# Performance work log

Measured on AMD Instinct MI355X. Metric: run time of the kernel, lower is better.

## Reference

```python
import jax, jax.numpy as jnp
import numpy as np

SHRINK_THRES = 0.0025
EPS = 1e-12  # F.normalize default eps


def _l2norm(v, axis=-1):
    return v / jnp.maximum(jnp.linalg.norm(v, axis=axis, keepdims=True), EPS)


def setup_inputs() -> dict:
    key = jax.random.key(0)
    ks = jax.random.split(key, 5)
    N, C, H, W = 16, 256, 64, 64
    mem_dim = 512
    x = jax.random.normal(ks[0], (N, C, H, W), dtype=jnp.float32)
    memory = jax.random.normal(ks[1], (mem_dim, C), dtype=jnp.float32) * 0.1
    memory = _l2norm(memory, axis=1)
    w1 = jax.random.normal(ks[2], (C, C // 2), dtype=jnp.float32) * (1.0 / np.sqrt(C))
    b1 = jnp.zeros((C // 2,), dtype=jnp.float32)
    w2 = jax.random.normal(ks[3], (C // 2, C), dtype=jnp.float32) * (1.0 / np.sqrt(C // 2))
    b2 = jnp.zeros((C,), dtype=jnp.float32)
    return {"x": x, "memory": memory, "w1": w1, "b1": b1, "w2": w2, "b2": b2}


def reference(x, memory, w1, b1, w2, b2):
    N, C, H, W = x.shape
    # [N,C,H,W] -> [N*H*W, C]
    x_flat = jnp.transpose(x, (0, 2, 3, 1)).reshape(-1, C)
    x_norm = _l2norm(x_flat, axis=1)
    # shared MLP over memory slots: Linear -> ReLU -> Linear -> ReLU
    m = jax.nn.relu(memory @ w1 + b1)
    m = jax.nn.relu(m @ w2 + b2)
    mem_norm = _l2norm(m, axis=1)  # [M, C]
    # cosine similarity + softmax over memory slots
    att = jax.nn.softmax(x_norm @ mem_norm.T, axis=1)  # [N*H*W, M]
    # hard shrink + L1 renormalization
    att = jax.nn.relu(att - SHRINK_THRES)
    att = att / jnp.maximum(jnp.sum(att, axis=1, keepdims=True), EPS)
    out_flat = att @ mem_norm  # [N*H*W, C]
    output = jnp.transpose(out_flat.reshape(N, H, W, C), (0, 3, 1, 2))
    att_map = jnp.transpose(att.reshape(N, H, W, -1), (0, 3, 1, 2))
    return output, att_map
```

## Files before the change

kernel.cpp:

```cpp
#include <hip/hip_runtime.h>
#include <hip/hip_bf16.h>

typedef _Float16 half8 __attribute__((ext_vector_type(8)));
typedef _Float16 half4v __attribute__((ext_vector_type(4)));
typedef float floatx4 __attribute__((ext_vector_type(4)));

#define C_DIM 256
#define M_DIM 512
#define HW 4096
#define TAU 0.0025f
#define LCAP 96

__global__ __launch_bounds__(128) void prep_kernel(
    const float* __restrict__ memory, const float* __restrict__ w1,
    const float* __restrict__ b1, const float* __restrict__ w2,
    const float* __restrict__ b2,
    _Float16* __restrict__ mN, float* __restrict__ mN32)
{
  __shared__ float sm[256];
  __shared__ float sh[128];
  __shared__ float s_part[2];
  __shared__ float s_tot;
  const int r = blockIdx.x;
  const int t = threadIdx.x;
  sm[t]       = memory[r * C_DIM + t];
  sm[t + 128] = memory[r * C_DIM + t + 128];
  __syncthreads();
  float acc = b1[t];
#pragma unroll 8
  for (int c = 0; c < 256; ++c) acc = fmaf(sm[c], w1[c * 128 + t], acc);
  sh[t] = fmaxf(acc, 0.f);
  __syncthreads();
  float o0 = b2[t], o1 = b2[t + 128];
#pragma unroll 8
  for (int k = 0; k < 128; ++k) {
    float h = sh[k];
    o0 = fmaf(h, w2[k * 256 + t], o0);
    o1 = fmaf(h, w2[k * 256 + t + 128], o1);
  }
  o0 = fmaxf(o0, 0.f);
  o1 = fmaxf(o1, 0.f);
  float ss = o0 * o0 + o1 * o1;
#pragma unroll
  for (int off = 32; off >= 1; off >>= 1) ss += __shfl_down(ss, off);
  if ((t & 63) == 0) s_part[t >> 6] = ss;
  __syncthreads();
  if (t == 0) s_tot = s_part[0] + s_part[1];
  __syncthreads();
  const float inv = 1.f / fmaxf(sqrtf(s_tot), 1e-12f);
  const float v0 = o0 * inv, v1 = o1 * inv;
  mN[r * C_DIM + t]        = (_Float16)v0;
  mN[r * C_DIM + t + 128]  = (_Float16)v1;
  mN32[r * C_DIM + t]       = v0;
  mN32[r * C_DIM + t + 128] = v1;
}

__global__ __launch_bounds__(256) void zero_kernel(float* __restrict__ p)
{
  const size_t n4 = (size_t)16 * M_DIM * HW / 4;
  size_t i = (size_t)blockIdx.x * 256 + threadIdx.x;
  const size_t stride = (size_t)gridDim.x * 256;
  const floatx4 z = {0.f, 0.f, 0.f, 0.f};
  for (; i < n4; i += stride) ((floatx4*)p)[i] = z;
}

#define MFMA16(a, b, c) __builtin_amdgcn_mfma_f32_16x16x32_f16(a, b, c, 0, 0, 0)

__global__ __launch_bounds__(512, 4) void main_kernel(
    const float* __restrict__ x,
    const _Float16* __restrict__ mN,
    const float* __restrict__ mN32,
    float* __restrict__ out, float* __restrict__ attmap)
{
  __shared__ _Float16       Xh[64][264];
  __shared__ unsigned short s_lslot[64][LCAP];
  __shared__ float          s_lval[64][LCAP];
  __shared__ int      s_cnt[64];
  __shared__ float    s_sumsq[64];
  __shared__ float    s_sum1[64];
  __shared__ float    s_sum2[64];

  const int tid  = threadIdx.x;
  const int wave = tid >> 6;
  const int lane = tid & 63;
  const int q    = lane >> 4;
  const int c16  = lane & 15;
  const int g    = tid >> 3;
  const int pxq  = tid & 7;

  const int blk = blockIdx.x;
  const int img = blk >> 6;
  const int hw0 = (blk & 63) * 64;
  const float* __restrict__ xb = x + (size_t)img * C_DIM * HW + hw0;

  if (tid < 64) {
    s_sumsq[tid] = 0.f; s_sum1[tid] = 0.f; s_sum2[tid] = 0.f; s_cnt[tid] = 0;
  }
  __syncthreads();

#pragma unroll
  for (int h = 0; h < 2; ++h) {
    floatx4 v[4];
#pragma unroll
    for (int i = 0; i < 4; ++i)
      v[i] = *(const floatx4*)(xb + (size_t)(4 * g + i) * HW + (pxq + 8 * h) * 4);
    float ps[4];
#pragma unroll
    for (int j = 0; j < 4; ++j) {
      const int p = (pxq + 8 * h) * 4 + j;
      half4v hv = {(_Float16)v[0][j], (_Float16)v[1][j], (_Float16)v[2][j], (_Float16)v[3][j]};
      *(half4v*)&Xh[p][4 * g] = hv;
      ps[j] = v[0][j] * v[0][j] + v[1][j] * v[1][j] + v[2][j] * v[2][j] + v[3][j] * v[3][j];
    }
#pragma unroll
    for (int off = 8; off < 64; off <<= 1)
#pragma unroll
      for (int j = 0; j < 4; ++j) ps[j] += __shfl_xor(ps[j], off);
    if ((lane >> 3) == 0) {
#pragma unroll
      for (int j = 0; j < 4; ++j) atomicAdd(&s_sumsq[4 * (lane & 7) + 32 * h + j], ps[j]);
    }
  }

  const _Float16* bp[4];
#pragma unroll
  for (int nt = 0; nt < 4; ++nt)
    bp[nt] = mN + (size_t)(wave * 64 + nt * 16 + c16) * C_DIM + q * 8;
  half8 bcur[4], bnxt[4];
#pragma unroll
  for (int nt = 0; nt < 4; ++nt) bcur[nt] = *(const half8*)bp[nt];

  __syncthreads();

  floatx4 acc[4][4];
#pragma unroll
  for (int mt = 0; mt < 4; ++mt)
#pragma unroll
    for (int nt = 0; nt < 4; ++nt) {
      floatx4 z = {0.f, 0.f, 0.f, 0.f};
      acc[mt][nt] = z;
    }
#pragma unroll
  for (int kb = 0; kb < 8; ++kb) {
    if (kb < 7) {
#pragma unroll
      for (int nt = 0; nt < 4; ++nt) bnxt[nt] = *(const half8*)(bp[nt] + (kb + 1) * 32);
    }
    const int k0 = kb * 32 + q * 8;
    half8 ah[4];
#pragma unroll
    for (int mt = 0; mt < 4; ++mt) ah[mt] = *(const half8*)&Xh[mt * 16 + c16][k0];
#pragma unroll
    for (int nt = 0; nt < 4; ++nt)
#pragma unroll
      for (int mt = 0; mt < 4; ++mt)
        acc[mt][nt] = MFMA16(ah[mt], bcur[nt], acc[mt][nt]);
#pragma unroll
    for (int nt = 0; nt < 4; ++nt) bcur[nt] = bnxt[nt];
  }

#pragma unroll
  for (int mt = 0; mt < 4; ++mt)
#pragma unroll
    for (int r = 0; r < 4; ++r) {
      const int m = mt * 16 + q * 4 + r;
      const float iv = 1.f / fmaxf(sqrtf(s_sumsq[m]), 1e-12f);
      float s = 0.f;
#pragma unroll
      for (int nt = 0; nt < 4; ++nt) {
        const float e = __expf(acc[mt][nt][r] * iv);
        acc[mt][nt][r] = e;
        s += e;
      }
      s += __shfl_xor(s, 1);
      s += __shfl_xor(s, 2);
      s += __shfl_xor(s, 4);
      s += __shfl_xor(s, 8);
      if (c16 == 0) atomicAdd(&s_sum1[m], s);
    }
  __syncthreads();

#pragma unroll
  for (int mt = 0; mt < 4; ++mt)
#pragma unroll
    for (int r = 0; r < 4; ++r) {
      const int m = mt * 16 + q * 4 + r;
      const float isum = 1.f / s_sum1[m];
      float s = 0.f;
#pragma unroll
      for (int nt = 0; nt < 4; ++nt) {
        const float tv = fmaxf(acc[mt][nt][r] * isum - TAU, 0.f);
        acc[mt][nt][r] = tv;
        s += tv;
      }
      s += __shfl_xor(s, 1);
      s += __shfl_xor(s, 2);
      s += __shfl_xor(s, 4);
      s += __shfl_xor(s, 8);
      if (c16 == 0) atomicAdd(&s_sum2[m], s);
    }
  __syncthreads();

#pragma unroll
  for (int mt = 0; mt < 4; ++mt) {
    float rs[4];
#pragma unroll
    for (int r = 0; r < 4; ++r)
      rs[r] = 1.f / fmaxf(s_sum2[mt * 16 + q * 4 + r], 1e-12f);
#pragma unroll
    for (int nt = 0; nt < 4; ++nt) {
      floatx4 a4 = acc[mt][nt];
      const unsigned n = wave * 64 + nt * 16 + c16;
#pragma unroll
      for (int r = 0; r < 4; ++r) {
        a4[r] *= rs[r];
        if (a4[r] > 0.f) {
          const int m = mt * 16 + q * 4 + r;
          const int idx = atomicAdd(&s_cnt[m], 1);
          if (idx < LCAP) {
            s_lslot[m][idx] = (unsigned short)n;
            s_lval[m][idx]  = a4[r];
          }
          attmap[((size_t)img * M_DIM + n) * HW + hw0 + m] = a4[r];
        }
      }
    }
  }
  __syncthreads();

  const int px  = lane;
  const int chc = wave;
  const int cn  = min(s_cnt[px], LCAP);
  floatx4 f[8] = {{0.f,0.f,0.f,0.f},{0.f,0.f,0.f,0.f},{0.f,0.f,0.f,0.f},{0.f,0.f,0.f,0.f},
                  {0.f,0.f,0.f,0.f},{0.f,0.f,0.f,0.f},{0.f,0.f,0.f,0.f},{0.f,0.f,0.f,0.f}};
  for (int j = 0; j < cn; ++j) {
    const int slot  = s_lslot[px][j];
    const float v   = s_lval[px][j];
    const floatx4* row = (const floatx4*)(mN32 + (size_t)slot * C_DIM + chc * 32);
#pragma unroll
    for (int u = 0; u < 8; ++u) f[u] += v * row[u];
  }

#pragma unroll
  for (int cc = 0; cc < 32; ++cc)
    out[((size_t)img * C_DIM + chc * 32 + cc) * HW + hw0 + px] = f[cc >> 2][cc & 3];
}

extern "C" void kernel_launch(void* const* d_in, const int* in_sizes, int n_in,
                              void* d_out, int out_size, void* d_ws, size_t ws_size,
                              hipStream_t stream) {
  (void)in_sizes; (void)n_in; (void)out_size; (void)ws_size;
  const float* x      = (const float*)d_in[0];
  const float* memory = (const float*)d_in[1];
  const float* w1     = (const float*)d_in[2];
  const float* b1     = (const float*)d_in[3];
  const float* w2     = (const float*)d_in[4];
  const float* b2     = (const float*)d_in[5];
  float* out    = (float*)d_out;
  float* attmap = out + (size_t)16 * C_DIM * HW;

  _Float16* mN   = (_Float16*)d_ws;
  float*    mN32 = (float*)((char*)d_ws + (size_t)M_DIM * C_DIM * sizeof(_Float16));

  hipLaunchKernelGGL(prep_kernel, dim3(M_DIM), dim3(128), 0, stream,
                     memory, w1, b1, w2, b2, mN, mN32);
  hipLaunchKernelGGL(zero_kernel, dim3(2048), dim3(256), 0, stream, attmap);
  hipLaunchKernelGGL(main_kernel, dim3(1024), dim3(512), 0, stream,
                     x, mN, mN32, out, attmap);
}
```

Before: 326.4 us.

## Fold attmap zeroing into prep kernel and vectorize output gather stores

Removes the separate zero_kernel and has each prep_kernel thread zero a strided slice of the attention map, saving one kernel launch. It also remaps the final gather stage so each thread handles 4 consecutive pixels and 8 channels, giving float4 stores to out instead of scalar per-pixel stores. The trade-off is more serial work per prep block (512 blocks x 128 threads writing 128 float4 each). The new gather also loops over each of its 4 pixels' slot lists in turn, with less parallelism per thread.

After: 325.6 us (median of 2 runs). No clear change (-0.3%).

```diff
diff --git a/kernel.cpp b/kernel.cpp
--- a/kernel.cpp
+++ b/kernel.cpp
@@ -15,7 +15,8 @@
     const float* __restrict__ memory, const float* __restrict__ w1,
     const float* __restrict__ b1, const float* __restrict__ w2,
     const float* __restrict__ b2,
-    _Float16* __restrict__ mN, float* __restrict__ mN32)
+    _Float16* __restrict__ mN, float* __restrict__ mN32,
+    float* __restrict__ attmap)
 {
   __shared__ float sm[256];
   __shared__ float sh[128];
@@ -23,6 +24,15 @@
   __shared__ float s_tot;
   const int r = blockIdx.x;
   const int t = threadIdx.x;
+
+  {
+    const floatx4 z = {0.f, 0.f, 0.f, 0.f};
+    floatx4* p4 = (floatx4*)attmap;
+    size_t i = (size_t)r * 128 + t;
+#pragma unroll 4
+    for (int k = 0; k < 128; ++k) { p4[i] = z; i += 65536; }
+  }
+
   sm[t]       = memory[r * C_DIM + t];
   sm[t + 128] = memory[r * C_DIM + t + 128];
   __syncthreads();
@@ -53,15 +63,6 @@
   mN[r * C_DIM + t + 128]  = (_Float16)v1;
   mN32[r * C_DIM + t]       = v0;
   mN32[r * C_DIM + t + 128] = v1;
-}
-
-__global__ __launch_bounds__(256) void zero_kernel(float* __restrict__ p)
-{
-  const size_t n4 = (size_t)16 * M_DIM * HW / 4;
-  size_t i = (size_t)blockIdx.x * 256 + threadIdx.x;
-  const size_t stride = (size_t)gridDim.x * 256;
-  const floatx4 z = {0.f, 0.f, 0.f, 0.f};
-  for (; i < n4; i += stride) ((floatx4*)p)[i] = z;
 }
 
 #define MFMA16(a, b, c) __builtin_amdgcn_mfma_f32_16x16x32_f16(a, b, c, 0, 0, 0)
@@ -228,22 +229,28 @@
   }
   __syncthreads();
 
-  const int px  = lane;
-  const int chc = wave;
-  const int cn  = min(s_cnt[px], LCAP);
+  const int px4 = (tid & 15) * 4;
+  const int chg = tid >> 4;
   floatx4 f[8] = {{0.f,0.f,0.f,0.f},{0.f,0.f,0.f,0.f},{0.f,0.f,0.f,0.f},{0.f,0.f,0.f,0.f},
                   {0.f,0.f,0.f,0.f},{0.f,0.f,0.f,0.f},{0.f,0.f,0.f,0.f},{0.f,0.f,0.f,0.f}};
-  for (int j = 0; j < cn; ++j) {
-    const int slot  = s_lslot[px][j];
-    const float v   = s_lval[px][j];
-    const floatx4* row = (const floatx4*)(mN32 + (size_t)slot * C_DIM + chc * 32);
-#pragma unroll
-    for (int u = 0; u < 8; ++u) f[u] += v * row[u];
-  }
-
-#pragma unroll
-  for (int cc = 0; cc < 32; ++cc)
-    out[((size_t)img * C_DIM + chc * 32 + cc) * HW + hw0 + px] = f[cc >> 2][cc & 3];
+#pragma unroll
+  for (int p = 0; p < 4; ++p) {
+    const int cn = min(s_cnt[px4 + p], LCAP);
+    for (int j = 0; j < cn; ++j) {
+      const int slot  = s_lslot[px4 + p][j];
+      const float v   = s_lval[px4 + p][j];
+      const floatx4* row = (const floatx4*)(mN32 + (size_t)slot * C_DIM + chg * 8);
+      const floatx4 r0 = row[0], r1 = row[1];
+      f[0][p] += v * r0[0]; f[1][p] += v * r0[1];
+      f[2][p] += v * r0[2]; f[3][p] += v * r0[3];
+      f[4][p] += v * r1[0]; f[5][p] += v * r1[1];
+      f[6][p] += v * r1[2]; f[7][p] += v * r1[3];
+    }
+  }
+
+#pragma unroll
+  for (int c = 0; c < 8; ++c)
+    *(floatx4*)(out + ((size_t)img * C_DIM + chg * 8 + c) * HW + hw0 + px4) = f[c];
 }
 
 extern "C" void kernel_launch(void* const* d_in, const int* in_sizes, int n_in,
@@ -263,8 +270,7 @@
   float*    mN32 = (float*)((char*)d_ws + (size_t)M_DIM * C_DIM * sizeof(_Float16));
 
   hipLaunchKernelGGL(prep_kernel, dim3(M_DIM), dim3(128), 0, stream,
-                     memory, w1, b1, w2, b2, mN, mN32);
-  hipLaunchKernelGGL(zero_kernel, dim3(2048), dim3(256), 0, stream, attmap);
+                     memory, w1, b1, w2, b2, mN, mN32, attmap);
   hipLaunchKernelGGL(main_kernel, dim3(1024), dim3(512), 0, stream,
                      x, mN, mN32, out, attmap);
 }
```
